# Kernel optimization log

Measured on AMD Instinct MI355X. Metric: run time of the kernel, lower is better.

Reference implementation:

```python
import jax, jax.numpy as jnp
import numpy as np

B, D_FEAT, D_ATTR, N_CLS = 512, 2048, 312, 150


def setup_inputs() -> dict:
    key = jax.random.key(0)
    k1, k2, k3, k4, k5 = jax.random.split(key, 5)
    return {
        "x_f": jax.random.normal(k1, (B, D_FEAT), dtype=jnp.float32),
        "W": jax.random.normal(k2, (D_FEAT, D_ATTR), dtype=jnp.float32) * 0.02,
        "b": jax.random.normal(k3, (D_ATTR,), dtype=jnp.float32) * 0.02,
        "seen_att": jax.random.normal(k4, (N_CLS, D_ATTR), dtype=jnp.float32),
        "x_labels": jax.random.randint(k5, (B,), 0, N_CLS, dtype=jnp.int64),
    }


def reference(x_f, W, b, seen_att, x_labels):
    temp = 1.0
    pre_attr = x_f @ W + b                                # [B, D]
    log_p = jax.nn.log_softmax(pre_attr / temp, axis=-1)  # log pre_attr_softmax
    log_g = jax.nn.log_softmax(seen_att[x_labels] / temp, axis=-1)
    g = jnp.exp(log_g)                                    # gt_attr_softmax [B, D]

    # pairwise KL(target = g_i/g_j || input_logits = log(p_i/p_j)), reduction='sum':
    #   sum_d t * (log t - log_ratio_p)
    t_ratio = g[:, None, :] / g[None, :, :]                               # [B, B, D]
    log_t = log_g[:, None, :] - log_g[None, :, :]                         # [B, B, D]
    log_r = log_p[:, None, :] - log_p[None, :, :]                         # [B, B, D]
    kl = jnp.sum(t_ratio * (log_t - log_r), axis=-1)                      # [B, B]

    same = x_labels[:, None] == x_labels[None, :]
    upper = jnp.triu(jnp.ones((x_labels.shape[0],) * 2, dtype=bool), k=1)
    mask = same & upper

    count = jnp.sum(mask)
    loss = jnp.sum(jnp.where(mask, kl, 0.0))
    return jnp.where(count > 0, loss / count.astype(loss.dtype), loss)
```

## Files before the change

### kernel.cpp

```cpp
#include <hip/hip_runtime.h>
#include <math.h>

#define B      512
#define DF     2048
#define DA     312
#define NTHR   320
#define RT     8
#define KSPLIT 16
#define NRG    (B / RT)

__device__ __forceinline__ float wave_max_f(float v) {
  #pragma unroll
  for (int off = 32; off >= 1; off >>= 1)
    v = fmaxf(v, __shfl_down(v, off));
  return v;
}

__device__ __forceinline__ double wave_sum_d(double v) {
  #pragma unroll
  for (int off = 32; off >= 1; off >>= 1)
    v += __shfl_down(v, off);
  return v;
}

__device__ __forceinline__ void dev_store_d(double* p, double v) {
  __hip_atomic_store(p, v, __ATOMIC_RELAXED, __HIP_MEMORY_SCOPE_AGENT);
}
__device__ __forceinline__ double dev_load_d(const double* p) {
  return __hip_atomic_load(p, __ATOMIC_RELAXED, __HIP_MEMORY_SCOPE_AGENT);
}
__device__ __forceinline__ void dev_store_i(int* p, int v) {
  __hip_atomic_store(p, v, __ATOMIC_RELAXED, __HIP_MEMORY_SCOPE_AGENT);
}
__device__ __forceinline__ int dev_load_i(const int* p) {
  return __hip_atomic_load(p, __ATOMIC_RELAXED, __HIP_MEMORY_SCOPE_AGENT);
}

template <int KC>
__global__ __launch_bounds__(NTHR, 5) void gemm_partial_kernel(
    const float* __restrict__ x_f, const float* __restrict__ W,
    float* __restrict__ part, int* ticket) {
  const int c    = threadIdx.x;
  const int rg   = blockIdx.x;
  const int ks   = blockIdx.y;
  const int row0 = rg * RT;
  const int k0   = ks * KC;
  const int ksplit = DF / KC;

  if (blockIdx.x == 0 && blockIdx.y == 0 && threadIdx.x == 0)
    *ticket = 0;

  if (c >= DA) return;

  float acc[RT];
  #pragma unroll
  for (int r = 0; r < RT; ++r) acc[r] = 0.f;

  const float* Wp = W + (size_t)k0 * DA + c;
  const float* xp = x_f + (size_t)row0 * DF + k0;

  float wc[8];
  #pragma unroll
  for (int j = 0; j < 8; ++j) wc[j] = Wp[(size_t)j * DA];

  #pragma unroll
  for (int k = 0; k < KC; k += 8) {
    float wn[8];
    if (k + 8 < KC) {
      #pragma unroll
      for (int j = 0; j < 8; ++j) wn[j] = Wp[(size_t)(k + 8 + j) * DA];
    }
    #pragma unroll
    for (int r = 0; r < RT; ++r) {
      const float* xr = xp + (size_t)r * DF + k;
      #pragma unroll
      for (int j = 0; j < 8; ++j) acc[r] = fmaf(xr[j], wc[j], acc[r]);
    }
    if (k + 8 < KC) {
      #pragma unroll
      for (int j = 0; j < 8; ++j) wc[j] = wn[j];
    }
  }

  float* pp = part + ((size_t)(rg * ksplit + ks) * RT) * DA + c;
  #pragma unroll
  for (int r = 0; r < RT; ++r) pp[(size_t)r * DA] = acc[r];
}

template <int KS>
__global__ __launch_bounds__(NTHR) void rowstats_pair_kernel(
    const float* __restrict__ part, const float* __restrict__ b,
    const int* __restrict__ labels,
    double* T, int* RK, int* ticket, float* __restrict__ out) {
  __shared__ float  red_f[8];
  __shared__ double red_d[16];
  __shared__ int    red_i[16];
  __shared__ float  bcast_max;
  __shared__ int    ticket_sh;
  __shared__ int    Lsh[B];

  const int tid  = threadIdx.x;
  const int wid  = tid >> 6;
  const int lane = tid & 63;
  const int row  = blockIdx.x;
  const int rg   = row / RT;
  const int r    = row & (RT - 1);

  for (int i = tid; i < B; i += NTHR) Lsh[i] = labels[i];

  float v = -INFINITY;
  float ps[KS];
  const bool active = (tid < DA);
  if (active) {
    const float* pb = part + ((size_t)(rg * KS) * RT + r) * DA + tid;
    #pragma unroll
    for (int p = 0; p < KS; ++p) ps[p] = pb[(size_t)p * RT * DA];
  }

  __syncthreads();

  const int myl = Lsh[row];
  int c_less = 0, c_all = 0;
  for (int j = tid; j < B; j += NTHR) {
    const int same = (Lsh[j] == myl) ? 1 : 0;
    c_all += same;
    if (j < row) c_less += same;
  }
  #pragma unroll
  for (int off = 32; off >= 1; off >>= 1) {
    c_less += __shfl_down(c_less, off);
    c_all  += __shfl_down(c_all,  off);
  }
  if (lane == 0) { red_i[wid] = c_less; red_i[8 + wid] = c_all; }

  if (active) {
    float s = b[tid];
    #pragma unroll
    for (int p = 0; p < KS; ++p) s += ps[p];
    v = s;
  }

  float m = wave_max_f(v);
  if (lane == 0) red_f[wid] = m;
  __syncthreads();
  if (tid == 0) {
    float mm = red_f[0];
    #pragma unroll
    for (int w = 1; w < NTHR / 64; ++w) mm = fmaxf(mm, red_f[w]);
    bcast_max = mm;
  }
  __syncthreads();
  const float rowmax = bcast_max;

  double e  = active ? exp((double)v - (double)rowmax) : 0.0;
  double sp = active ? (double)v : 0.0;
  double es = wave_sum_d(e);
  double ss = wave_sum_d(sp);
  if (lane == 0) { red_d[wid] = es; red_d[8 + wid] = ss; }
  __syncthreads();
  if (tid == 0) {
    double esum = 0.0, ssum = 0.0;
    int rank = 0, mcnt = 0;
    #pragma unroll
    for (int w = 0; w < NTHR / 64; ++w) {
      esum += red_d[w]; ssum += red_d[8 + w];
      rank += red_i[w]; mcnt += red_i[8 + w];
    }
    const double S    = ssum - (double)DA * ((double)rowmax + log(esum));
    const double coef = (double)(2 * rank - mcnt + 1);
    dev_store_d(&T[row], coef * S);
    dev_store_i(&RK[row], rank);
  }

  asm volatile("s_waitcnt vmcnt(0)" ::: "memory");
  __syncthreads();
  if (tid == 0)
    ticket_sh = __hip_atomic_fetch_add(ticket, 1, __ATOMIC_RELAXED,
                                       __HIP_MEMORY_SCOPE_AGENT);
  __syncthreads();
  if (ticket_sh != B - 1) return;
  asm volatile("" ::: "memory");

  double tloc = 0.0;
  int    rloc = 0;
  for (int i = tid; i < B; i += NTHR) {
    tloc += dev_load_d(&T[i]);
    rloc += dev_load_i(&RK[i]);
  }
  #pragma unroll
  for (int off = 32; off >= 1; off >>= 1) {
    tloc += __shfl_down(tloc, off);
    rloc += __shfl_down(rloc, off);
  }
  if (lane == 0) { red_d[wid] = tloc; red_i[wid] = rloc; }
  __syncthreads();
  if (tid == 0) {
    double ts = 0.0; int rs = 0;
    #pragma unroll
    for (int w = 0; w < NTHR / 64; ++w) { ts += red_d[w]; rs += red_i[w]; }
    out[0] = (float)((rs > 0) ? ts / (double)rs : ts);
  }
}

template <int KCF>
__global__ __launch_bounds__(NTHR) void gemm_partial_fb(
    const float* __restrict__ x_f, const float* __restrict__ W,
    float* __restrict__ part) {
  const int c = threadIdx.x, rg = blockIdx.x, ks = blockIdx.y;
  const int row0 = rg * RT, k0 = ks * KCF, ksplit = DF / KCF;
  if (c >= DA) return;
  float acc[RT];
  #pragma unroll
  for (int r = 0; r < RT; ++r) acc[r] = 0.f;
  const float* Wp = W + (size_t)k0 * DA + c;
  const float* xp = x_f + (size_t)row0 * DF + k0;
  for (int k = 0; k < KCF; k += 8) {
    float w[8];
    #pragma unroll
    for (int j = 0; j < 8; ++j) w[j] = Wp[(size_t)(k + j) * DA];
    #pragma unroll
    for (int r = 0; r < RT; ++r) {
      const float* xr = xp + (size_t)r * DF + k;
      #pragma unroll
      for (int j = 0; j < 8; ++j) acc[r] = fmaf(xr[j], w[j], acc[r]);
    }
  }
  float* pp = part + ((size_t)(rg * ksplit + ks) * RT) * DA + c;
  #pragma unroll
  for (int r = 0; r < RT; ++r) pp[(size_t)r * DA] = acc[r];
}

template <int KS>
__global__ __launch_bounds__(NTHR) void row_stats_fb(
    const float* __restrict__ part, const float* __restrict__ b,
    double* __restrict__ S) {
  __shared__ float  red_f[8];
  __shared__ double red_d[16];
  __shared__ float  bcast_max;
  const int tid = threadIdx.x, wid = tid >> 6, lane = tid & 63;
  const int row = blockIdx.x, rg = row / RT, r = row & (RT - 1);
  float v = -INFINITY;
  if (tid < DA) {
    const float* pb = part + ((size_t)(rg * KS) * RT + r) * DA + tid;
    float ps[KS];
    #pragma unroll
    for (int p = 0; p < KS; ++p) ps[p] = pb[(size_t)p * RT * DA];
    float sv = b[tid];
    #pragma unroll
    for (int p = 0; p < KS; ++p) sv += ps[p];
    v = sv;
  }
  float m = wave_max_f(v);
  if (lane == 0) red_f[wid] = m;
  __syncthreads();
  if (tid == 0) {
    float mm = red_f[0];
    #pragma unroll
    for (int w = 1; w < NTHR / 64; ++w) mm = fmaxf(mm, red_f[w]);
    bcast_max = mm;
  }
  __syncthreads();
  const float rowmax = bcast_max;
  double e  = (tid < DA) ? exp((double)v - (double)rowmax) : 0.0;
  double sp = (tid < DA) ? (double)v : 0.0;
  double es = wave_sum_d(e);
  double ss = wave_sum_d(sp);
  if (lane == 0) { red_d[wid] = es; red_d[8 + wid] = ss; }
  __syncthreads();
  if (tid == 0) {
    double esum = 0.0, ssum = 0.0;
    #pragma unroll
    for (int w = 0; w < NTHR / 64; ++w) { esum += red_d[w]; ssum += red_d[8 + w]; }
    S[row] = ssum - (double)DA * ((double)rowmax + log(esum));
  }
}

__global__ __launch_bounds__(1024) void pair_reduce_fb(
    const double* __restrict__ S, const int* __restrict__ labels,
    float* __restrict__ out) {
  __shared__ double    Ss[B];
  __shared__ int       Ls[B];
  __shared__ double    red_d[16];
  __shared__ long long red_i[16];
  const int tid = threadIdx.x;
  if (tid < B) { Ss[tid] = S[tid]; Ls[tid] = labels[tid]; }
  __syncthreads();
  double lsum = 0.0;
  long long lcnt = 0;
  for (int p = tid; p < B * B; p += 1024) {
    int i = p >> 9, j = p & (B - 1);
    if (j > i && Ls[i] == Ls[j]) { lsum += Ss[j] - Ss[i]; lcnt++; }
  }
  #pragma unroll
  for (int off = 32; off >= 1; off >>= 1) {
    lsum += __shfl_down(lsum, off);
    lcnt += __shfl_down(lcnt, off);
  }
  const int wid = tid >> 6, lane = tid & 63;
  if (lane == 0) { red_d[wid] = lsum; red_i[wid] = lcnt; }
  __syncthreads();
  if (tid == 0) {
    double s = 0.0; long long c = 0;
    #pragma unroll
    for (int w = 0; w < 16; ++w) { s += red_d[w]; c += red_i[w]; }
    out[0] = (float)((c > 0) ? s / (double)c : s);
  }
}

extern "C" void kernel_launch(void* const* d_in, const int* in_sizes, int n_in,
                              void* d_out, int out_size, void* d_ws, size_t ws_size,
                              hipStream_t stream) {
  const float* x_f    = (const float*)d_in[0];
  const float* W      = (const float*)d_in[1];
  const float* b      = (const float*)d_in[2];
  const int*   labels = (const int*)d_in[4];

  const size_t need = 16384 + (size_t)KSPLIT * B * DA * 4;
  if (ws_size >= need) {
    int*    ticket = (int*)d_ws;
    double* T      = (double*)((char*)d_ws + 4096);
    int*    RK     = (int*)((char*)d_ws + 8192);
    float*  part   = (float*)((char*)d_ws + 16384);
    dim3 g1(NRG, KSPLIT);
    gemm_partial_kernel<DF / KSPLIT><<<g1, NTHR, 0, stream>>>(x_f, W, part,
                                                              ticket);
    rowstats_pair_kernel<KSPLIT><<<B, NTHR, 0, stream>>>(
        part, b, labels, T, RK, ticket, (float*)d_out);
  } else {
    double* S    = (double*)d_ws;
    float*  part = (float*)((char*)d_ws + 4096);
    dim3 g1(NRG, 2);
    gemm_partial_fb<DF / 2><<<g1, NTHR, 0, stream>>>(x_f, W, part);
    row_stats_fb<2><<<B, NTHR, 0, stream>>>(part, b, S);
    pair_reduce_fb<<<1, 1024, 0, stream>>>(S, labels, (float*)d_out);
  }
}
```

Baseline: 93.94 us.

## Stage W tiles through double-buffered shared memory with float4 loads in GEMM

The split-K GEMM now loads each 16-row slab of W into a double-buffered LDS tile using coalesced float4 loads from all threads, and prefetches the next slab into registers while computing the current one. Each column thread then reads W from LDS instead of issuing strided scalar global loads. This is meant to cut global load instruction count and improve coalescing, at the cost of about 40KB of LDS per block, which may reduce occupancy under launch_bounds(320,5), and an extra barrier per chunk.

Measured after the change: 135.6 us. 1.44x slower.

```diff
diff --git a/kernel.cpp b/kernel.cpp
--- a/kernel.cpp
+++ b/kernel.cpp
@@ -8,6 +8,7 @@
 #define RT     8
 #define KSPLIT 16
 #define NRG    (B / RT)
+#define TK     16
 
 __device__ __forceinline__ float wave_max_f(float v) {
   #pragma unroll
@@ -40,51 +41,91 @@
 __global__ __launch_bounds__(NTHR, 5) void gemm_partial_kernel(
     const float* __restrict__ x_f, const float* __restrict__ W,
     float* __restrict__ part, int* ticket) {
-  const int c    = threadIdx.x;
+  constexpr int NCH = KC / TK;
+  constexpr int NF4 = TK * DA / 4;
+  __shared__ __align__(16) float wbuf[2][TK * DA];
+
+  const int tid  = threadIdx.x;
+  const int c    = tid;
   const int rg   = blockIdx.x;
   const int ks   = blockIdx.y;
   const int row0 = rg * RT;
   const int k0   = ks * KC;
   const int ksplit = DF / KC;
-
-  if (blockIdx.x == 0 && blockIdx.y == 0 && threadIdx.x == 0)
+  const bool active = (c < DA);
+
+  if (blockIdx.x == 0 && blockIdx.y == 0 && tid == 0)
     *ticket = 0;
 
-  if (c >= DA) return;
+  const float* wsrc = W + (size_t)k0 * DA;
+  const float* xp   = x_f + (size_t)row0 * DF + k0;
 
   float acc[RT];
   #pragma unroll
   for (int r = 0; r < RT; ++r) acc[r] = 0.f;
 
-  const float* Wp = W + (size_t)k0 * DA + c;
-  const float* xp = x_f + (size_t)row0 * DF + k0;
-
-  float wc[8];
-  #pragma unroll
-  for (int j = 0; j < 8; ++j) wc[j] = Wp[(size_t)j * DA];
-
-  #pragma unroll
-  for (int k = 0; k < KC; k += 8) {
-    float wn[8];
-    if (k + 8 < KC) {
+  float4 ld[4];
+
+  {
+    const float4* s = (const float4*)wsrc;
+    #pragma unroll
+    for (int rd = 0; rd < 4; ++rd) {
+      const int idx = rd * NTHR + tid;
+      if (idx < NF4) ld[rd] = s[idx];
+    }
+    float4* d = (float4*)wbuf[0];
+    #pragma unroll
+    for (int rd = 0; rd < 4; ++rd) {
+      const int idx = rd * NTHR + tid;
+      if (idx < NF4) d[idx] = ld[rd];
+    }
+  }
+  __syncthreads();
+
+  for (int ch = 0; ch < NCH; ++ch) {
+    const int cur = ch & 1;
+
+    if (ch + 1 < NCH) {
+      const float4* s = (const float4*)(wsrc + (size_t)(ch + 1) * TK * DA);
       #pragma unroll
-      for (int j = 0; j < 8; ++j) wn[j] = Wp[(size_t)(k + 8 + j) * DA];
-    }
-    #pragma unroll
-    for (int r = 0; r < RT; ++r) {
-      const float* xr = xp + (size_t)r * DF + k;
+      for (int rd = 0; rd < 4; ++rd) {
+        const int idx = rd * NTHR + tid;
+        if (idx < NF4) ld[rd] = s[idx];
+      }
+    }
+
+    if (active) {
       #pragma unroll
-      for (int j = 0; j < 8; ++j) acc[r] = fmaf(xr[j], wc[j], acc[r]);
-    }
-    if (k + 8 < KC) {
+      for (int o = 0; o < TK / 8; ++o) {
+        const int kk = ch * TK + o * 8;
+        float wv[8];
+        #pragma unroll
+        for (int j = 0; j < 8; ++j) wv[j] = wbuf[cur][(o * 8 + j) * DA + c];
+        #pragma unroll
+        for (int r = 0; r < RT; ++r) {
+          const float* xr = xp + (size_t)r * DF + kk;
+          #pragma unroll
+          for (int j = 0; j < 8; ++j) acc[r] = fmaf(xr[j], wv[j], acc[r]);
+        }
+      }
+    }
+
+    if (ch + 1 < NCH) {
+      float4* d = (float4*)wbuf[(ch + 1) & 1];
       #pragma unroll
-      for (int j = 0; j < 8; ++j) wc[j] = wn[j];
-    }
-  }
-
-  float* pp = part + ((size_t)(rg * ksplit + ks) * RT) * DA + c;
-  #pragma unroll
-  for (int r = 0; r < RT; ++r) pp[(size_t)r * DA] = acc[r];
+      for (int rd = 0; rd < 4; ++rd) {
+        const int idx = rd * NTHR + tid;
+        if (idx < NF4) d[idx] = ld[rd];
+      }
+    }
+    __syncthreads();
+  }
+
+  if (active) {
+    float* pp = part + ((size_t)(rg * ksplit + ks) * RT) * DA + c;
+    #pragma unroll
+    for (int r = 0; r < RT; ++r) pp[(size_t)r * DA] = acc[r];
+  }
 }
 
 template <int KS>
@@ -329,7 +370,7 @@
   } else {
     double* S    = (double*)d_ws;
     float*  part = (float*)((char*)d_ws + 4096);
-    dim3 g1(NRG, 2);
+    dim3 g1(B / RT, 2);
     gemm_partial_fb<DF / 2><<<g1, NTHR, 0, stream>>>(x_f, W, part);
     row_stats_fb<2><<<B, NTHR, 0, stream>>>(part, b, S);
     pair_reduce_fb<<<1, 1024, 0, stream>>>(S, labels, (float*)d_out);
```
